# Kernel tuning notes

Measured on AMD Instinct MI355X. Metric: run time of the kernel, lower is better.

The kernel has to match this reference:

```python
import jax, jax.numpy as jnp
import numpy as np

B, S, D_MODEL, H = 2, 2048, 1024, 16
HD = D_MODEL // H  # 64
EPS = 1e-6


def setup_inputs() -> dict:
    key = jax.random.key(0)
    ks = jax.random.split(key, 8)
    x = jax.random.normal(ks[0], (B, S, D_MODEL), dtype=jnp.float32)
    # Proper RoPE rotation angles: theta_i = pos / 10000^(2i/head_dim)
    inv_freq = 1.0 / (10000.0 ** (np.arange(0, HD, 2, dtype=np.float32) / HD))  # (HD/2,)
    angles = np.arange(S, dtype=np.float32)[:, None] * inv_freq[None, :]        # (S, HD/2)
    rope_cos = jnp.asarray(np.cos(angles))
    rope_sin = jnp.asarray(np.sin(angles))
    w_std = 1.0 / np.sqrt(D_MODEL)
    wq = jax.random.normal(ks[1], (D_MODEL, D_MODEL), dtype=jnp.float32) * w_std
    wk = jax.random.normal(ks[2], (D_MODEL, D_MODEL), dtype=jnp.float32) * w_std
    wv = jax.random.normal(ks[3], (D_MODEL, D_MODEL), dtype=jnp.float32) * w_std
    wo = jax.random.normal(ks[4], (D_MODEL, D_MODEL), dtype=jnp.float32) * w_std
    q_scale = 1.0 + 0.02 * jax.random.normal(ks[5], (HD,), dtype=jnp.float32)
    k_scale = 1.0 + 0.02 * jax.random.normal(ks[6], (HD,), dtype=jnp.float32)
    return {"x": x, "wq": wq, "wk": wk, "wv": wv, "wo": wo,
            "q_scale": q_scale, "k_scale": k_scale,
            "rope_cos": rope_cos, "rope_sin": rope_sin}


def _rmsnorm(t, scale):
    # RMSNorm over head_dim
    var = jnp.mean(jnp.square(t), axis=-1, keepdims=True)
    return t * jax.lax.rsqrt(var + EPS) * scale


def _apply_rope(t, cos, sin):
    # t: (B,S,H,HD); interpret consecutive pairs as complex (real, imag)
    b, s, h, d = t.shape
    tp = t.reshape(b, s, h, d // 2, 2)
    tr, ti = tp[..., 0], tp[..., 1]
    c = cos[None, :, None, :]  # (1,S,1,HD/2)
    sn = sin[None, :, None, :]
    or_ = tr * c - ti * sn
    oi = tr * sn + ti * c
    return jnp.stack([or_, oi], axis=-1).reshape(b, s, h, d)


def reference(x, wq, wk, wv, wo, q_scale, k_scale, rope_cos, rope_sin):
    b, s, _ = x.shape
    # Torch-style linear: y = x @ W^T, W is (out, in)
    q = jnp.einsum('bsd,od->bso', x, wq).reshape(b, s, H, HD)
    k = jnp.einsum('bsd,od->bso', x, wk).reshape(b, s, H, HD)
    v = jnp.einsum('bsd,od->bso', x, wv).reshape(b, s, H, HD)
    q = _apply_rope(_rmsnorm(q, q_scale), rope_cos, rope_sin)
    k = _apply_rope(_rmsnorm(k, k_scale), rope_cos, rope_sin)
    # scaled dot-product attention (no mask), fp32 softmax
    scale = 1.0 / np.sqrt(HD)
    scores = jnp.einsum('bqhd,bkhd->bhqk', q, k) * scale
    probs = jax.nn.softmax(scores.astype(jnp.float32), axis=-1)
    attn = jnp.einsum('bhqk,bkhd->bqhd', probs, v).reshape(b, s, D_MODEL)
    return jnp.einsum('bso,do->bsd', attn, wo.T).astype(x.dtype) if False else jnp.einsum('bsd,od->bso', attn, wo)
```

## Files before the change

### kernel.cpp

```cpp
#include <hip/hip_runtime.h>
#include <hip/hip_bf16.h>


#define B_ 2
#define S_ 2048
#define D_ 1024
#define H_ 16
#define HD_ 64
#define M_ (B_*S_)
#define SPLIT_ 4
#define KSPAN_ (S_/SPLIT_)

typedef __attribute__((ext_vector_type(8))) short short8;
typedef __attribute__((ext_vector_type(4))) short short4v;
typedef __attribute__((ext_vector_type(4))) float f32x4;
typedef __attribute__((ext_vector_type(4))) _Float16 half4;
typedef __attribute__((ext_vector_type(8))) _Float16 half8;

static __device__ __forceinline__ short f2bf(float f) {
    __hip_bfloat16 h = __float2bfloat16(f);
    return *reinterpret_cast<short*>(&h);
}
static __device__ __forceinline__ short f2h(float f) {
    _Float16 h = (_Float16)f;
    return *reinterpret_cast<short*>(&h);
}
static __device__ __forceinline__ float bf2f(short s) {
    unsigned u = ((unsigned)(unsigned short)s) << 16;
    float f; __builtin_memcpy(&f, &u, 4); return f;
}

typedef __attribute__((address_space(1))) const unsigned int gu32_t;
typedef __attribute__((address_space(3))) unsigned int lu32_t;
static __device__ __forceinline__ void gld16(const short* g, short* l) {
    __builtin_amdgcn_global_load_lds((gu32_t*)g, (lu32_t*)l, 16, 0, 0);
}

__global__ __launch_bounds__(256)
void convert_bf16(const float* __restrict__ x,
                  const float* __restrict__ wq, const float* __restrict__ wk,
                  const float* __restrict__ wv, const float* __restrict__ wo,
                  short* __restrict__ xb, short* __restrict__ wqkvb, short* __restrict__ wob)
{
    const size_t t4 = ((size_t)blockIdx.x * 256 + threadIdx.x) * 4;
    const float* src; short* dst; size_t off, doff;
    if (t4 < 4194304)      { src = x;  dst = xb;    off = t4;           doff = t4; }
    else if (t4 < 5242880) { src = wq; dst = wqkvb; off = t4 - 4194304; doff = t4 - 4194304; }
    else if (t4 < 6291456) { src = wk; dst = wqkvb; off = t4 - 5242880; doff = t4 - 4194304; }
    else if (t4 < 7340032) { src = wv; dst = wqkvb; off = t4 - 6291456; doff = t4 - 4194304; }
    else                   { src = wo; dst = wob;   off = t4 - 7340032; doff = t4 - 7340032; }
    float4 v = *(const float4*)(src + off);
    short4v s = { f2bf(v.x), f2bf(v.y), f2bf(v.z), f2bf(v.w) };
    *(short4v*)(dst + doff) = s;
}

__global__ __launch_bounds__(256)
void gemm_qkv(const short* __restrict__ A, const short* __restrict__ Bw,
              short* __restrict__ Qb, short* __restrict__ Kb, short* __restrict__ Vt)
{
    __shared__ __align__(16) short As[128*32];
    __shared__ __align__(16) short Bs[128*32];
    const int tid = threadIdx.x;
    const int w = tid >> 6, lane = tid & 63, quad = lane >> 4, l16 = lane & 15;
    const int wr = w >> 1, wc = w & 1;
    const int bm0 = blockIdx.x * 128, bn0 = blockIdx.y * 128;

    const int srow = tid >> 2;
    const int skch = (tid & 3) * 8;
    const short* gA0 = A  + (size_t)(bm0 + srow) * 1024 + skch;
    const short* gA1 = A  + (size_t)(bm0 + 64 + srow) * 1024 + skch;
    const short* gB0 = Bw + (size_t)(bn0 + srow) * 1024 + skch;
    const short* gB1 = Bw + (size_t)(bn0 + 64 + srow) * 1024 + skch;
    short* lA0 = As + w*512;
    short* lA1 = As + 2048 + w*512;
    short* lB0 = Bs + w*512;
    short* lB1 = Bs + 2048 + w*512;

    f32x4 acc[4][4];
    #pragma unroll
    for (int i = 0; i < 4; ++i)
        #pragma unroll
        for (int j = 0; j < 4; ++j) acc[i][j] = (f32x4){0.f,0.f,0.f,0.f};

    for (int k0 = 0; k0 < 1024; k0 += 32) {
        __syncthreads();
        gld16(gA0 + k0, lA0);
        gld16(gA1 + k0, lA1);
        gld16(gB0 + k0, lB0);
        gld16(gB1 + k0, lB1);
        __syncthreads();
        short8 af[4], bfr[4];
        #pragma unroll
        for (int i = 0; i < 4; ++i)
            af[i] = *(const short8*)(As + (wr*64 + i*16 + l16)*32 + quad*8);
        #pragma unroll
        for (int j = 0; j < 4; ++j)
            bfr[j] = *(const short8*)(Bs + (wc*64 + j*16 + l16)*32 + quad*8);
        #pragma unroll
        for (int i = 0; i < 4; ++i)
            #pragma unroll
            for (int j = 0; j < 4; ++j)
                acc[i][j] = __builtin_amdgcn_mfma_f32_16x16x32_bf16(af[i], bfr[j], acc[i][j], 0, 0, 0);
    }

    #pragma unroll
    for (int i = 0; i < 4; ++i) {
        #pragma unroll
        for (int r = 0; r < 4; ++r) {
            const int m = bm0 + wr*64 + i*16 + quad*4 + r;
            #pragma unroll
            for (int j = 0; j < 4; ++j) {
                const int n = bn0 + wc*64 + j*16 + l16;
                const float v = acc[i][j][r];
                const int which = n >> 10, nn = n & 1023;
                const int h = nn >> 6, hd = nn & 63;
                const int b = m >> 11, s = m & (S_-1);
                if (which == 0)      Qb[(((size_t)b*H_ + h)*S_ + s)*HD_ + hd] = f2bf(v);
                else if (which == 1) Kb[(((size_t)b*H_ + h)*S_ + s)*HD_ + hd] = f2bf(v);
                else                 Vt[(((size_t)b*H_ + h)*HD_ + hd)*S_ + s] = f2h(v);
            }
        }
    }
}

__global__ __launch_bounds__(256)
void gemm_out(const short* __restrict__ po, const float* __restrict__ pl,
              const short* __restrict__ Bw, float* __restrict__ C)
{
    __shared__ __align__(16) short As[64*32];
    __shared__ __align__(16) short Bs[128*32];
    const int tid = threadIdx.x;
    const int w = tid >> 6, lane = tid & 63, quad = lane >> 4, l16 = lane & 15;
    const int bm0 = blockIdx.x * 64, bn0 = blockIdx.y * 128;

    const int srow = tid >> 2;
    const int skch = (tid & 3) * 8;
    const int m = bm0 + srow;
    const int b = m >> 11, s = m & (S_-1);
    const short* gB0 = Bw + (size_t)(bn0 + srow) * 1024 + skch;
    const short* gB1 = Bw + (size_t)(bn0 + 64 + srow) * 1024 + skch;
    short* lB0 = Bs + w*512;
    short* lB1 = Bs + 2048 + w*512;

    float inv[16];
    #pragma unroll
    for (int h = 0; h < 16; ++h) {
        float l = 0.f;
        #pragma unroll
        for (int sp = 0; sp < SPLIT_; ++sp)
            l += pl[(size_t)sp*65536 + ((size_t)(b*16 + h))*S_ + s];
        inv[h] = 1.0f / l;
    }

    f32x4 acc[4][2];
    #pragma unroll
    for (int i = 0; i < 4; ++i) {
        acc[i][0] = (f32x4){0.f,0.f,0.f,0.f};
        acc[i][1] = (f32x4){0.f,0.f,0.f,0.f};
    }

    for (int k0 = 0; k0 < 1024; k0 += 32) {
        const int h = k0 >> 6;
        half8 p0 = *(const half8*)(po + 0ull*4194304 + (size_t)m*1024 + k0 + skch);
        half8 p1 = *(const half8*)(po + 1ull*4194304 + (size_t)m*1024 + k0 + skch);
        half8 p2 = *(const half8*)(po + 2ull*4194304 + (size_t)m*1024 + k0 + skch);
        half8 p3 = *(const half8*)(po + 3ull*4194304 + (size_t)m*1024 + k0 + skch);
        short8 a;
        #pragma unroll
        for (int j = 0; j < 8; ++j)
            a[j] = f2bf((((float)p0[j] + (float)p1[j]) + ((float)p2[j] + (float)p3[j])) * inv[h]);
        __syncthreads();
        *(short8*)(As + srow*32 + skch) = a;
        gld16(gB0 + k0, lB0);
        gld16(gB1 + k0, lB1);
        __syncthreads();
        short8 af[4], bfr[2];
        #pragma unroll
        for (int i = 0; i < 4; ++i)
            af[i] = *(const short8*)(As + (i*16 + l16)*32 + quad*8);
        #pragma unroll
        for (int j = 0; j < 2; ++j)
            bfr[j] = *(const short8*)(Bs + (w*32 + j*16 + l16)*32 + quad*8);
        #pragma unroll
        for (int i = 0; i < 4; ++i)
            #pragma unroll
            for (int j = 0; j < 2; ++j)
                acc[i][j] = __builtin_amdgcn_mfma_f32_16x16x32_bf16(af[i], bfr[j], acc[i][j], 0, 0, 0);
    }

    #pragma unroll
    for (int i = 0; i < 4; ++i)
        #pragma unroll
        for (int r = 0; r < 4; ++r) {
            const int mm = bm0 + i*16 + quad*4 + r;
            #pragma unroll
            for (int j = 0; j < 2; ++j) {
                const int n = bn0 + w*32 + j*16 + l16;
                C[(size_t)mm*1024 + n] = acc[i][j][r];
            }
        }
}

__global__ __launch_bounds__(256)
void rmsnorm_rope(short* __restrict__ qbh, short* __restrict__ kbh,
                  const float* __restrict__ q_scale, const float* __restrict__ k_scale,
                  const float* __restrict__ rope_cos, const float* __restrict__ rope_sin)
{
    const int lane = threadIdx.x & 63;
    const int wid  = threadIdx.x >> 6;
    const int row  = blockIdx.x * 4 + wid;
    const bool isq = (blockIdx.y == 0);
    short* t = isq ? qbh : kbh;
    const float* sc = isq ? q_scale : k_scale;
    const int s = row & (S_-1);
    float v = bf2f(t[(size_t)row * HD_ + lane]);
    float ssum = v * v;
    #pragma unroll
    for (int m = 32; m >= 1; m >>= 1) ssum += __shfl_xor(ssum, m, 64);
    float r = rsqrtf(ssum * (1.0f/64.0f) + 1e-6f);
    float nv = v * r * sc[lane];
    const int p = lane >> 1;
    float c  = rope_cos[s*32 + p];
    float sn = rope_sin[s*32 + p];
    float partner = __shfl_xor(nv, 1, 64);
    float outv = (lane & 1) ? (partner * sn + nv * c) : (nv * c - partner * sn);
    if (isq) outv *= 0.18033688011112042f;
    t[(size_t)row * HD_ + lane] = f2bf(outv);
}

__global__ __launch_bounds__(256)
void flash_mfma(const short* __restrict__ qb, const short* __restrict__ kb,
                const short* __restrict__ vt, short* __restrict__ po, float* __restrict__ pl)
{
    __shared__ __align__(16) short Ks[64*64];
    __shared__ __align__(16) short Vs[64*64];

    const int id   = blockIdx.x;
    const int xcd  = id & 7;
    const int rest = id >> 3;
    const int qblk = rest & 15;
    const int g    = (rest >> 4) * 8 + xcd;
    const int bh   = g >> 2;
    const int sp   = g & 3;

    const int tid  = threadIdx.x;
    const int wv   = tid >> 6;
    const int lane = tid & 63;
    const int quad = lane >> 4;
    const int l16  = lane & 15;
    const int b    = bh >> 4, h = bh & (H_-1);
    const int q0   = qblk * 128 + wv * 32;
    const int kt0  = sp * KSPAN_;
    const size_t hbase = (size_t)bh * S_ * HD_;
    const size_t vbase = (size_t)bh * HD_ * S_;
    short* po_sp = po + (size_t)sp * 4194304;
    float* pl_sp = pl + (size_t)sp * 65536;

    const int c0r = tid >> 3,       c0c = tid & 7;
    const int c1r = (tid+256) >> 3, c1c = (tid+256) & 7;

    short8 qfrag[2][2];
    #pragma unroll
    for (int qf = 0; qf < 2; ++qf)
        #pragma unroll
        for (int c = 0; c < 2; ++c)
            qfrag[qf][c] = *(const short8*)(qb + hbase + (size_t)(q0 + qf*16 + l16)*HD_ + c*32 + quad*8);

    f32x4 Oacc[2][4];
    #pragma unroll
    for (int qf = 0; qf < 2; ++qf)
        #pragma unroll
        for (int dt = 0; dt < 4; ++dt) Oacc[qf][dt] = (f32x4){0.f,0.f,0.f,0.f};
    float l_lane[2] = {0.f, 0.f};

    short8 rk0 = *(const short8*)(kb + hbase + (size_t)(kt0 + c0r)*HD_ + c0c*8);
    short8 rk1 = *(const short8*)(kb + hbase + (size_t)(kt0 + c1r)*HD_ + c1c*8);
    short8 rv0 = *(const short8*)(vt + vbase + (size_t)c0r*S_ + kt0 + c0c*8);
    short8 rv1 = *(const short8*)(vt + vbase + (size_t)c1r*S_ + kt0 + c1c*8);

    #pragma unroll 1
    for (int t = 0; t < KSPAN_/64; ++t) {
        __syncthreads();
        *(short8*)(Ks + c0r*64 + ((c0c ^ (c0r & 7)) << 3)) = rk0;
        *(short8*)(Ks + c1r*64 + ((c1c ^ (c1r & 7)) << 3)) = rk1;
        *(short8*)(Vs + c0r*64 + ((c0c ^ (c0r & 7)) << 3)) = rv0;
        *(short8*)(Vs + c1r*64 + ((c1c ^ (c1r & 7)) << 3)) = rv1;
        __syncthreads();
        if (t < KSPAN_/64 - 1) {
            const int ktn = kt0 + (t+1)*64;
            rk0 = *(const short8*)(kb + hbase + (size_t)(ktn + c0r)*HD_ + c0c*8);
            rk1 = *(const short8*)(kb + hbase + (size_t)(ktn + c1r)*HD_ + c1c*8);
            rv0 = *(const short8*)(vt + vbase + (size_t)c0r*S_ + ktn + c0c*8);
            rv1 = *(const short8*)(vt + vbase + (size_t)c1r*S_ + ktn + c1c*8);
        }

        #pragma unroll
        for (int st = 0; st < 4; ++st) {
            short8 kf0 = *(const short8*)(Ks + (st*16 + l16)*64 + (((quad    ) ^ (l16 & 7)) << 3));
            short8 kf1 = *(const short8*)(Ks + (st*16 + l16)*64 + (((4 + quad) ^ (l16 & 7)) << 3));
            const int ch16 = st*2 + (quad >> 1);
            const int sw   = ((ch16 ^ (l16 & 7)) << 3) + (quad & 1)*4;
            half4 va[4];
            #pragma unroll
            for (int dt = 0; dt < 4; ++dt)
                va[dt] = *(const half4*)(Vs + (dt*16 + l16)*64 + sw);
            #pragma unroll
            for (int qf = 0; qf < 2; ++qf) {
                f32x4 acc = (f32x4){0.f,0.f,0.f,0.f};
                acc = __builtin_amdgcn_mfma_f32_16x16x32_bf16(kf0, qfrag[qf][0], acc, 0, 0, 0);
                acc = __builtin_amdgcn_mfma_f32_16x16x32_bf16(kf1, qfrag[qf][1], acc, 0, 0, 0);
                half4 pb;
                #pragma unroll
                for (int r = 0; r < 4; ++r) {
                    float p = __builtin_amdgcn_exp2f(acc[r] - 12.0f);
                    l_lane[qf] += p;
                    pb[r] = (_Float16)p;
                }
                #pragma unroll
                for (int dt = 0; dt < 4; ++dt)
                    Oacc[qf][dt] = __builtin_amdgcn_mfma_f32_16x16x16f16(va[dt], pb, Oacc[qf][dt], 0, 0, 0);
            }
        }
    }

    #pragma unroll
    for (int qf = 0; qf < 2; ++qf) {
        l_lane[qf] += __shfl_xor(l_lane[qf], 16, 64);
        l_lane[qf] += __shfl_xor(l_lane[qf], 32, 64);
        if (quad == 0) pl_sp[(size_t)bh*S_ + q0 + qf*16 + l16] = l_lane[qf];
    }
    #pragma unroll
    for (int qf = 0; qf < 2; ++qf) {
        const int s = q0 + qf*16 + l16;
        #pragma unroll
        for (int dt = 0; dt < 4; ++dt) {
            short4v o;
            #pragma unroll
            for (int r = 0; r < 4; ++r) o[r] = f2h(Oacc[qf][dt][r]);
            *(short4v*)(po_sp + (((size_t)b*S_ + s)*H_ + h)*HD_ + dt*16 + quad*4) = o;
        }
    }
}

extern "C" void kernel_launch(void* const* d_in, const int* in_sizes, int n_in,
                              void* d_out, int out_size, void* d_ws, size_t ws_size,
                              hipStream_t stream)
{
    (void)in_sizes; (void)n_in; (void)out_size; (void)ws_size;
    const float* x        = (const float*)d_in[0];
    const float* wq       = (const float*)d_in[1];
    const float* wk       = (const float*)d_in[2];
    const float* wv       = (const float*)d_in[3];
    const float* wo       = (const float*)d_in[4];
    const float* q_scale  = (const float*)d_in[5];
    const float* k_scale  = (const float*)d_in[6];
    const float* rope_cos = (const float*)d_in[7];
    const float* rope_sin = (const float*)d_in[8];
    float* out = (float*)d_out;
    short* ws  = (short*)d_ws;

    short* qbh   = ws;
    short* kbh   = ws + 4194304;
    short* vt    = ws + 8388608;
    short* xb    = ws + 16777216;
    short* wqkvb = ws + 20971520;
    short* wob   = ws + 24117248;
    short* po    = ws + 25165824;
    float* pl    = (float*)(ws + 41943040);

    convert_bf16<<<dim3(8192), 256, 0, stream>>>(x, wq, wk, wv, wo, xb, wqkvb, wob);
    gemm_qkv<<<dim3(M_/128, 24), 256, 0, stream>>>(xb, wqkvb, qbh, kbh, vt);
    rmsnorm_rope<<<dim3(B_*H_*S_/4, 2), 256, 0, stream>>>(qbh, kbh, q_scale, k_scale, rope_cos, rope_sin);
    flash_mfma<<<dim3((S_/128)*B_*H_*SPLIT_), 256, 0, stream>>>(qbh, kbh, vt, po, pl);
    gemm_out<<<dim3(M_/64, D_/128), 256, 0, stream>>>(po, pl, wob, out);
}
```

Before: 231.5 us.

## Fuse RMSNorm and RoPE into QKV GEMM epilogue and halve attention KV split

The separate rmsnorm_rope kernel is removed. Its per-head normalization and rotary embedding now run in the epilogue of the QKV GEMM, using lane shuffles across the 16-lane groups that hold one head row. The flash-attention split-K factor drops from 4 to 2, which halves the partial outputs the output GEMM has to read and combine. The cost is half as many flash blocks, so less parallelism, and a heavier GEMM epilogue with scattered cos/sin loads.

```diff
diff --git a/kernel.cpp b/kernel.cpp
--- a/kernel.cpp
+++ b/kernel.cpp
@@ -8,7 +8,7 @@
 #define H_ 16
 #define HD_ 64
 #define M_ (B_*S_)
-#define SPLIT_ 4
+#define SPLIT_ 2
 #define KSPAN_ (S_/SPLIT_)
 
 typedef __attribute__((ext_vector_type(8))) short short8;
@@ -24,10 +24,6 @@
 static __device__ __forceinline__ short f2h(float f) {
     _Float16 h = (_Float16)f;
     return *reinterpret_cast<short*>(&h);
-}
-static __device__ __forceinline__ float bf2f(short s) {
-    unsigned u = ((unsigned)(unsigned short)s) << 16;
-    float f; __builtin_memcpy(&f, &u, 4); return f;
 }
 
 typedef __attribute__((address_space(1))) const unsigned int gu32_t;
@@ -56,7 +52,9 @@
 
 __global__ __launch_bounds__(256)
 void gemm_qkv(const short* __restrict__ A, const short* __restrict__ Bw,
-              short* __restrict__ Qb, short* __restrict__ Kb, short* __restrict__ Vt)
+              short* __restrict__ Qb, short* __restrict__ Kb, short* __restrict__ Vt,
+              const float* __restrict__ q_scale, const float* __restrict__ k_scale,
+              const float* __restrict__ rope_cos, const float* __restrict__ rope_sin)
 {
     __shared__ __align__(16) short As[128*32];
     __shared__ __align__(16) short Bs[128*32];
@@ -103,23 +101,54 @@
                 acc[i][j] = __builtin_amdgcn_mfma_f32_16x16x32_bf16(af[i], bfr[j], acc[i][j], 0, 0, 0);
     }
 
-    #pragma unroll
-    for (int i = 0; i < 4; ++i) {
-        #pragma unroll
-        for (int r = 0; r < 4; ++r) {
-            const int m = bm0 + wr*64 + i*16 + quad*4 + r;
-            #pragma unroll
-            for (int j = 0; j < 4; ++j) {
-                const int n = bn0 + wc*64 + j*16 + l16;
-                const float v = acc[i][j][r];
-                const int which = n >> 10, nn = n & 1023;
-                const int h = nn >> 6, hd = nn & 63;
+    const int nbase = bn0 + wc*64;
+    const int which = nbase >> 10;
+    const int h     = (nbase & 1023) >> 6;
+
+    if (which < 2) {
+        const float* sc = which ? k_scale : q_scale;
+        short* dst      = which ? Kb : Qb;
+        const float fold = which ? 1.0f : 0.18033688011112042f;
+        float scv[4];
+        #pragma unroll
+        for (int j = 0; j < 4; ++j) scv[j] = sc[j*16 + l16];
+        #pragma unroll
+        for (int i = 0; i < 4; ++i) {
+            #pragma unroll
+            for (int r = 0; r < 4; ++r) {
+                const int m = bm0 + wr*64 + i*16 + quad*4 + r;
                 const int b = m >> 11, s = m & (S_-1);
-                if (which == 0)      Qb[(((size_t)b*H_ + h)*S_ + s)*HD_ + hd] = f2bf(v);
-                else if (which == 1) Kb[(((size_t)b*H_ + h)*S_ + s)*HD_ + hd] = f2bf(v);
-                else                 Vt[(((size_t)b*H_ + h)*HD_ + hd)*S_ + s] = f2h(v);
+                float ss = 0.f;
+                #pragma unroll
+                for (int j = 0; j < 4; ++j) ss += acc[i][j][r] * acc[i][j][r];
+                #pragma unroll
+                for (int msk = 1; msk <= 8; msk <<= 1) ss += __shfl_xor(ss, msk, 64);
+                const float rn = rsqrtf(ss * (1.0f/64.0f) + 1e-6f);
+                #pragma unroll
+                for (int j = 0; j < 4; ++j) {
+                    const int hd = j*16 + l16;
+                    const float nv = acc[i][j][r] * rn * scv[j];
+                    const float c  = rope_cos[s*32 + (hd >> 1)];
+                    const float sn = rope_sin[s*32 + (hd >> 1)];
+                    const float partner = __shfl_xor(nv, 1, 64);
+                    const float o = (hd & 1) ? (partner * sn + nv * c) : (nv * c - partner * sn);
+                    dst[(((size_t)b*H_ + h)*S_ + s)*HD_ + hd] = f2bf(o * fold);
+                }
             }
         }
+    } else {
+        #pragma unroll
+        for (int i = 0; i < 4; ++i)
+            #pragma unroll
+            for (int r = 0; r < 4; ++r) {
+                const int m = bm0 + wr*64 + i*16 + quad*4 + r;
+                const int b = m >> 11, s = m & (S_-1);
+                #pragma unroll
+                for (int j = 0; j < 4; ++j) {
+                    const int hd = j*16 + l16;
+                    Vt[(((size_t)b*H_ + h)*HD_ + hd)*S_ + s] = f2h(acc[i][j][r]);
+                }
+            }
     }
 }
 
@@ -144,13 +173,8 @@
 
     float inv[16];
     #pragma unroll
-    for (int h = 0; h < 16; ++h) {
-        float l = 0.f;
-        #pragma unroll
-        for (int sp = 0; sp < SPLIT_; ++sp)
-            l += pl[(size_t)sp*65536 + ((size_t)(b*16 + h))*S_ + s];
-        inv[h] = 1.0f / l;
-    }
+    for (int h = 0; h < 16; ++h)
+        inv[h] = 1.0f / (pl[((size_t)(b*16 + h))*S_ + s] + pl[65536 + ((size_t)(b*16 + h))*S_ + s]);
 
     f32x4 acc[4][2];
     #pragma unroll
@@ -161,14 +185,12 @@
 
     for (int k0 = 0; k0 < 1024; k0 += 32) {
         const int h = k0 >> 6;
-        half8 p0 = *(const half8*)(po + 0ull*4194304 + (size_t)m*1024 + k0 + skch);
-        half8 p1 = *(const half8*)(po + 1ull*4194304 + (size_t)m*1024 + k0 + skch);
-        half8 p2 = *(const half8*)(po + 2ull*4194304 + (size_t)m*1024 + k0 + skch);
-        half8 p3 = *(const half8*)(po + 3ull*4194304 + (size_t)m*1024 + k0 + skch);
+        half8 p0 = *(const half8*)(po +            (size_t)m*1024 + k0 + skch);
+        half8 p1 = *(const half8*)(po + 4194304 + (size_t)m*1024 + k0 + skch);
         short8 a;
         #pragma unroll
         for (int j = 0; j < 8; ++j)
-            a[j] = f2bf((((float)p0[j] + (float)p1[j]) + ((float)p2[j] + (float)p3[j])) * inv[h]);
+            a[j] = f2bf(((float)p0[j] + (float)p1[j]) * inv[h]);
         __syncthreads();
         *(short8*)(As + srow*32 + skch) = a;
         gld16(gB0 + k0, lB0);
@@ -199,33 +221,6 @@
                 C[(size_t)mm*1024 + n] = acc[i][j][r];
             }
         }
-}
-
-__global__ __launch_bounds__(256)
-void rmsnorm_rope(short* __restrict__ qbh, short* __restrict__ kbh,
-                  const float* __restrict__ q_scale, const float* __restrict__ k_scale,
-                  const float* __restrict__ rope_cos, const float* __restrict__ rope_sin)
-{
-    const int lane = threadIdx.x & 63;
-    const int wid  = threadIdx.x >> 6;
-    const int row  = blockIdx.x * 4 + wid;
-    const bool isq = (blockIdx.y == 0);
-    short* t = isq ? qbh : kbh;
-    const float* sc = isq ? q_scale : k_scale;
-    const int s = row & (S_-1);
-    float v = bf2f(t[(size_t)row * HD_ + lane]);
-    float ssum = v * v;
-    #pragma unroll
-    for (int m = 32; m >= 1; m >>= 1) ssum += __shfl_xor(ssum, m, 64);
-    float r = rsqrtf(ssum * (1.0f/64.0f) + 1e-6f);
-    float nv = v * r * sc[lane];
-    const int p = lane >> 1;
-    float c  = rope_cos[s*32 + p];
-    float sn = rope_sin[s*32 + p];
-    float partner = __shfl_xor(nv, 1, 64);
-    float outv = (lane & 1) ? (partner * sn + nv * c) : (nv * c - partner * sn);
-    if (isq) outv *= 0.18033688011112042f;
-    t[(size_t)row * HD_ + lane] = f2bf(outv);
 }
 
 __global__ __launch_bounds__(256)
@@ -240,8 +235,8 @@
     const int rest = id >> 3;
     const int qblk = rest & 15;
     const int g    = (rest >> 4) * 8 + xcd;
-    const int bh   = g >> 2;
-    const int sp   = g & 3;
+    const int bh   = g >> 1;
+    const int sp   = g & 1;
 
     const int tid  = threadIdx.x;
     const int wv   = tid >> 6;
@@ -366,11 +361,11 @@
     short* wqkvb = ws + 20971520;
     short* wob   = ws + 24117248;
     short* po    = ws + 25165824;
-    float* pl    = (float*)(ws + 41943040);
+    float* pl    = (float*)(ws + 33554432);
 
     convert_bf16<<<dim3(8192), 256, 0, stream>>>(x, wq, wk, wv, wo, xb, wqkvb, wob);
-    gemm_qkv<<<dim3(M_/128, 24), 256, 0, stream>>>(xb, wqkvb, qbh, kbh, vt);
-    rmsnorm_rope<<<dim3(B_*H_*S_/4, 2), 256, 0, stream>>>(qbh, kbh, q_scale, k_scale, rope_cos, rope_sin);
+    gemm_qkv<<<dim3(M_/128, 24), 256, 0, stream>>>(xb, wqkvb, qbh, kbh, vt,
+                                                   q_scale, k_scale, rope_cos, rope_sin);
     flash_mfma<<<dim3((S_/128)*B_*H_*SPLIT_), 256, 0, stream>>>(qbh, kbh, vt, po, pl);
     gemm_out<<<dim3(M_/64, D_/128), 256, 0, stream>>>(po, pl, wob, out);
 }
```

After: 211.0 us. 8.9% less time.
